# Optimization experiments

Measured on AMD Instinct MI355X. Metric: run time of the kernel, lower is better.

Reference implementation:

```python
import jax, jax.numpy as jnp
import numpy as np

RES_SIZE = 64
SR = 24000
MIN_FREQ = 10.0
MAX_FREQ = 12000.0
DECAY_FACTOR = 0.999
HIGH_FREQ_DECAY = 0.6


def _build_kernels():
    # Deterministic complex resonator bank from __init__ (registered buffer).
    freqs = np.logspace(np.log10(MIN_FREQ), np.log10(MAX_FREQ), RES_SIZE)
    decays = np.linspace(DECAY_FACTOR, HIGH_FREQ_DECAY, RES_SIZE)
    k_len = int(1.0 * SR)  # 24000
    t = np.arange(k_len)
    thetas = 2 * np.pi * freqs / SR
    eig = decays * np.exp(1j * thetas)  # (64,)
    kernels = eig[:, None] ** t[None, :]  # (64, 24000) complex
    kernels /= np.abs(kernels).sum(axis=1, keepdims=True)
    return kernels.astype(np.complex64)


def setup_inputs() -> dict:
    key = jax.random.key(0)
    audio = jax.random.normal(key, (8, 48000), dtype=jnp.float32)
    k = _build_kernels()
    return {
        "audio": audio,
        "kernels_re": jnp.asarray(k.real, dtype=jnp.float32),
        "kernels_im": jnp.asarray(k.imag, dtype=jnp.float32),
    }


def reference(audio, kernels_re, kernels_im):
    # audio: (B, T) float32; kernels: (C=64, K=24000) complex64 (as re/im pair)
    kernels = (kernels_re + 1j * kernels_im).astype(jnp.complex64)
    T = audio.shape[-1]
    K = kernels.shape[-1]
    n_fft = T + K - 1
    audio_c = audio.astype(jnp.complex64)

    ker_f = jnp.fft.fft(kernels, n=n_fft, axis=-1)[None, :, :]  # (1, C, n_fft)

    # forward-direction convolution
    sig_f = jnp.fft.fft(audio_c[:, None, :], n=n_fft, axis=-1)  # (B, 1, n_fft)
    out_f = jnp.fft.ifft(sig_f * ker_f, axis=-1)[..., :T]        # (B, C, T)

    # backward-direction convolution (time-reversed input, then re-reversed)
    sig_b = jnp.fft.fft(audio_c[:, ::-1][:, None, :], n=n_fft, axis=-1)
    out_b = jnp.fft.ifft(sig_b * ker_f, axis=-1)[..., :T][..., ::-1]

    # (B, 4*C, T): [RealF, ImagF, RealB, ImagB]
    return jnp.concatenate(
        [out_f.real, out_f.imag, out_b.real, out_b.imag], axis=1
    ).astype(jnp.float32)
```

## Files before the change

### kernel.cpp

```cpp
#include <hip/hip_runtime.h>

#define BATCH   8
#define NCH     64
#define TLEN    48000
#define KLEN    24000
#define NDIR    2
#define CHUNK   256
#define NCHUNK  188
#define NBD     (BATCH*NDIR)
#define NTASK_A (NBD*NCHUNK)
#define NTASK_C (NTASK_A*NCH)

#define WS_EIG_OFF ((size_t)NTASK_C * sizeof(float2))

__global__ __launch_bounds__(64) void pass0_eig(double* __restrict__ eig_out) {
    int c = threadIdx.x;
    if (c >= NCH) return;
    double fc  = (double)c / 63.0;
    double dec = 0.999 + (0.6 - 0.999) * fc;
    double lf  = 1.0 + (4.0791812460476247 - 1.0) * fc;
    double f   = pow(10.0, lf);
    double th  = 2.0 * 3.14159265358979323846 * f / 24000.0;
    eig_out[2 * c]     = dec * cos(th);
    eig_out[2 * c + 1] = dec * sin(th);
}

__global__ __launch_bounds__(256) void pass_a(const float* __restrict__ audio,
                                              const double* __restrict__ eig,
                                              float2* __restrict__ s_out) {
    int lane = threadIdx.x & 63;
    int task = blockIdx.x * 4 + (threadIdx.x >> 6);
    int chunk = task % NCHUNK;
    int bd    = task / NCHUNK;
    int d = bd & 1, b = bd >> 1;
    int c = lane;

    float er = (float)eig[2 * c], ei = (float)eig[2 * c + 1];
    float E2r = er * er - ei * ei, E2i = 2.f * er * ei;

    const float* ab = audio + b * TLEN;
    int base = chunk * CHUNK;
    int len  = min(CHUNK, TLEN - base);

    float sr = 0.f, si = 0.f;
    for (int t = 0; t < len; t += 2) {
        int u0 = base + t, u1 = base + t + 1;
        float x0 = ab[d ? (TLEN - 1 - u0) : u0];
        float x1 = ab[d ? (TLEN - 1 - u1) : u1];
        float wr = er * x0 + x1;
        float wi = ei * x0;
        float nr = E2r * sr - E2i * si + wr;
        float ni = E2r * si + E2i * sr + wi;
        sr = nr; si = ni;
    }
    s_out[task * NCH + c] = make_float2(sr, si);
}

__global__ __launch_bounds__(256) void pass_b(float2* __restrict__ buf,
                                              const double* __restrict__ eig) {
    int tid = blockIdx.x * 256 + threadIdx.x;
    if (tid >= NBD * NCH) return;
    int c  = tid & 63;
    int bd = tid >> 6;

    double er = eig[2 * c], ei = eig[2 * c + 1];
    double lr = er, li = ei;
    #pragma unroll
    for (int s = 0; s < 8; ++s) { double r = lr, i = li; lr = r * r - i * i; li = 2.0 * r * i; }

    double Sr = 0.0, Si = 0.0;
    #pragma unroll 4
    for (int i = 0; i < NCHUNK; ++i) {
        int idx = (bd * NCHUNK + i) * NCH + c;
        float2 s = buf[idx];
        buf[idx] = make_float2((float)Sr, (float)Si);
        double nr = lr * Sr - li * Si + (double)s.x;
        double ni = lr * Si + li * Sr + (double)s.y;
        Sr = nr; Si = ni;
    }
}

__global__ __launch_bounds__(256) void pass_c(const float* __restrict__ audio,
                                              const float* __restrict__ kre,
                                              const double* __restrict__ eig,
                                              const float2* __restrict__ S_in,
                                              float* __restrict__ out) {
    int lane = threadIdx.x & 63;
    int task = blockIdx.x * 4 + (threadIdx.x >> 6);
    int c     = task & 63;
    int tmp   = task >> 6;
    int chunk = tmp % NCHUNK;
    int bd    = tmp / NCHUNK;
    int d = bd & 1, b = bd >> 1;

    float Er[8], Ei[8];
    Er[0] = (float)eig[2 * c]; Ei[0] = (float)eig[2 * c + 1];
    #pragma unroll
    for (int s = 1; s < 8; ++s) {
        float r = Er[s - 1], i = Ei[s - 1];
        Er[s] = r * r - i * i; Ei[s] = 2.f * r * i;
    }
    float Qr = 1.f, Qi = 0.f;
    #pragma unroll
    for (int s = 0; s < 6; ++s) {
        float fr = Er[s + 2], fi = Ei[s + 2];
        float nr = Qr * fr - Qi * fi, ni = Qr * fi + Qi * fr;
        bool bit = (lane >> s) & 1;
        Qr = bit ? nr : Qr; Qi = bit ? ni : Qi;
    }
    float e1r = Er[0], e1i = Ei[0];
    float e2r = Er[1], e2i = Ei[1];
    float e3r = e1r * e2r - e1i * e2i, e3i = e1r * e2i + e1i * e2r;
    float e4r = Er[2], e4i = Ei[2];

    float  g  = kre[c * KLEN];
    float2 Sp = S_in[task];

    const float* ab = audio + b * TLEN;
    int base = chunk * CHUNK;
    int u    = base + 4 * lane;
    bool act = u < TLEN;

    float4 x;
    if (act) {
        if (!d) x = *(const float4*)(ab + u);
        else { float4 r = *(const float4*)(ab + (TLEN - 4 - u)); x = make_float4(r.w, r.z, r.y, r.x); }
    } else x = make_float4(0.f, 0.f, 0.f, 0.f);

    float z0r = x.x,                          z0i = 0.f;
    float z1r = e1r * z0r + x.y,              z1i = e1i * z0r;
    float z2r = e1r * z1r - e1i * z1i + x.z,  z2i = e1r * z1i + e1i * z1r;
    float z3r = e1r * z2r - e1i * z2i + x.w,  z3i = e1r * z2i + e1i * z2r;

    float Sr = z3r, Si = z3i;
    #pragma unroll
    for (int s = 0; s < 6; ++s) {
        float vr = __shfl_up(Sr, (unsigned)(1 << s), 64);
        float vi = __shfl_up(Si, (unsigned)(1 << s), 64);
        bool ok = lane >= (1 << s);
        vr = ok ? vr : 0.f; vi = ok ? vi : 0.f;
        float fr = Er[s + 2], fi = Ei[s + 2];
        Sr += fr * vr - fi * vi;
        Si += fr * vi + fi * vr;
    }
    float Cr = __shfl_up(Sr, 1u, 64), Ci = __shfl_up(Si, 1u, 64);
    if (lane == 0) { Cr = 0.f; Ci = 0.f; }
    float Dr = Cr + Qr * Sp.x - Qi * Sp.y;
    float Di = Ci + Qr * Sp.y + Qi * Sp.x;

    float y0r = z0r + e1r * Dr - e1i * Di, y0i = z0i + e1r * Di + e1i * Dr;
    float y1r = z1r + e2r * Dr - e2i * Di, y1i = z1i + e2r * Di + e2i * Dr;
    float y2r = z2r + e3r * Dr - e3i * Di, y2i = z2i + e3r * Di + e3i * Dr;
    float y3r = z3r + e4r * Dr - e4i * Di, y3i = z3i + e4r * Di + e4i * Dr;

    float* outR = out + (size_t)(b * 256 + d * 128 + c) * TLEN;
    float* outI = outR + (size_t)64 * TLEN;
    if (act) {
        if (!d) {
            *(float4*)(outR + u) = make_float4(g * y0r, g * y1r, g * y2r, g * y3r);
            *(float4*)(outI + u) = make_float4(g * y0i, g * y1i, g * y2i, g * y3i);
        } else {
            int p = TLEN - 4 - u;
            *(float4*)(outR + p) = make_float4(g * y3r, g * y2r, g * y1r, g * y0r);
            *(float4*)(outI + p) = make_float4(g * y3i, g * y2i, g * y1i, g * y0i);
        }
    }
}

extern "C" void kernel_launch(void* const* d_in, const int* in_sizes, int n_in,
                              void* d_out, int out_size, void* d_ws, size_t ws_size,
                              hipStream_t stream) {
    const float* audio = (const float*)d_in[0];
    const float* kre   = (const float*)d_in[1];
    float* out         = (float*)d_out;

    float2* ws_buf = (float2*)d_ws;
    double* ws_eig = (double*)((char*)d_ws + WS_EIG_OFF);

    pass0_eig<<<1, 64, 0, stream>>>(ws_eig);
    pass_a<<<NTASK_A / 4, 256, 0, stream>>>(audio, ws_eig, ws_buf);
    pass_b<<<(NBD * NCH + 255) / 256, 256, 0, stream>>>(ws_buf, ws_eig);
    pass_c<<<NTASK_C / 4, 256, 0, stream>>>(audio, kre, ws_eig, ws_buf, out);
}
```

Before: 453.6 us.

## Process four chunks per wave in pass_c with nontemporal output stores

Each pass_c wave now handles a super-chunk of four 256-sample chunks. It derives the carry-in for chunks 2-4 locally from the previous chunk's scan total and eig^256, so it no longer reads a separate carry per chunk. This spreads the eigen-power setup and the carry load over more work and gives each wave independent shuffle scans to interleave. Output writes use nontemporal stores to avoid polluting the cache with the large output, and pass_a's recurrence loop is unrolled. The costs are higher register pressure, a quarter as many waves, and some extra float rounding from chaining carries in single precision.

Result: faster. 437.8 us (-3.5%).

```diff
diff --git a/kernel.cpp b/kernel.cpp
--- a/kernel.cpp
+++ b/kernel.cpp
@@ -7,11 +7,21 @@
 #define NDIR    2
 #define CHUNK   256
 #define NCHUNK  188
+#define SUPER   4
+#define SCHUNK  (CHUNK*SUPER)
+#define NSUP    47
 #define NBD     (BATCH*NDIR)
 #define NTASK_A (NBD*NCHUNK)
-#define NTASK_C (NTASK_A*NCH)
-
-#define WS_EIG_OFF ((size_t)NTASK_C * sizeof(float2))
+#define NTASK_C (NBD*NSUP*NCH)
+
+#define WS_EIG_OFF ((size_t)(NTASK_A * NCH) * sizeof(float2))
+
+typedef float v4f __attribute__((ext_vector_type(4)));
+
+__device__ __forceinline__ void nt_store4(float* p, float a, float b, float c, float d) {
+    v4f v = {a, b, c, d};
+    __builtin_nontemporal_store(v, (v4f*)p);
+}
 
 __global__ __launch_bounds__(64) void pass0_eig(double* __restrict__ eig_out) {
     int c = threadIdx.x;
@@ -43,6 +53,7 @@
     int len  = min(CHUNK, TLEN - base);
 
     float sr = 0.f, si = 0.f;
+    #pragma unroll 4
     for (int t = 0; t < len; t += 2) {
         int u0 = base + t, u1 = base + t + 1;
         float x0 = ab[d ? (TLEN - 1 - u0) : u0];
@@ -87,10 +98,10 @@
                                               float* __restrict__ out) {
     int lane = threadIdx.x & 63;
     int task = blockIdx.x * 4 + (threadIdx.x >> 6);
-    int c     = task & 63;
-    int tmp   = task >> 6;
-    int chunk = tmp % NCHUNK;
-    int bd    = tmp / NCHUNK;
+    int c   = task & 63;
+    int tmp = task >> 6;
+    int sc  = tmp % NSUP;
+    int bd  = tmp / NSUP;
     int d = bd & 1, b = bd >> 1;
 
     float Er[8], Ei[8];
@@ -100,6 +111,9 @@
         float r = Er[s - 1], i = Ei[s - 1];
         Er[s] = r * r - i * i; Ei[s] = 2.f * r * i;
     }
+    float e256r = Er[7] * Er[7] - Ei[7] * Ei[7];
+    float e256i = 2.f * Er[7] * Ei[7];
+
     float Qr = 1.f, Qi = 0.f;
     #pragma unroll
     for (int s = 0; s < 6; ++s) {
@@ -114,55 +128,94 @@
     float e4r = Er[2], e4i = Ei[2];
 
     float  g  = kre[c * KLEN];
-    float2 Sp = S_in[task];
+    float2 Sp = S_in[(bd * NCHUNK + SUPER * sc) * NCH + c];
 
     const float* ab = audio + b * TLEN;
-    int base = chunk * CHUNK;
-    int u    = base + 4 * lane;
-    bool act = u < TLEN;
-
-    float4 x;
-    if (act) {
-        if (!d) x = *(const float4*)(ab + u);
-        else { float4 r = *(const float4*)(ab + (TLEN - 4 - u)); x = make_float4(r.w, r.z, r.y, r.x); }
-    } else x = make_float4(0.f, 0.f, 0.f, 0.f);
-
-    float z0r = x.x,                          z0i = 0.f;
-    float z1r = e1r * z0r + x.y,              z1i = e1i * z0r;
-    float z2r = e1r * z1r - e1i * z1i + x.z,  z2i = e1r * z1i + e1i * z1r;
-    float z3r = e1r * z2r - e1i * z2i + x.w,  z3i = e1r * z2i + e1i * z2r;
-
-    float Sr = z3r, Si = z3i;
+    int base0 = sc * SCHUNK;
+
+    float x0[SUPER], x1[SUPER], x2[SUPER], x3[SUPER];
+    bool  act[SUPER];
+    #pragma unroll
+    for (int j = 0; j < SUPER; ++j) {
+        int u = base0 + j * CHUNK + 4 * lane;
+        act[j] = (u < TLEN);
+        float4 x = make_float4(0.f, 0.f, 0.f, 0.f);
+        if (act[j]) {
+            if (!d) x = *(const float4*)(ab + u);
+            else { float4 r = *(const float4*)(ab + (TLEN - 4 - u)); x = make_float4(r.w, r.z, r.y, r.x); }
+        }
+        x0[j] = x.x; x1[j] = x.y; x2[j] = x.z; x3[j] = x.w;
+    }
+
+    float z0r[SUPER], z1r[SUPER], z1i[SUPER], z2r[SUPER], z2i[SUPER], z3r[SUPER], z3i[SUPER];
+    #pragma unroll
+    for (int j = 0; j < SUPER; ++j) {
+        z0r[j] = x0[j];
+        z1r[j] = e1r * z0r[j] + x1[j];
+        z1i[j] = e1i * z0r[j];
+        z2r[j] = e1r * z1r[j] - e1i * z1i[j] + x2[j];
+        z2i[j] = e1r * z1i[j] + e1i * z1r[j];
+        z3r[j] = e1r * z2r[j] - e1i * z2i[j] + x3[j];
+        z3i[j] = e1r * z2i[j] + e1i * z2r[j];
+    }
+
+    float Sr[SUPER], Si[SUPER];
+    #pragma unroll
+    for (int j = 0; j < SUPER; ++j) { Sr[j] = z3r[j]; Si[j] = z3i[j]; }
     #pragma unroll
     for (int s = 0; s < 6; ++s) {
-        float vr = __shfl_up(Sr, (unsigned)(1 << s), 64);
-        float vi = __shfl_up(Si, (unsigned)(1 << s), 64);
-        bool ok = lane >= (1 << s);
-        vr = ok ? vr : 0.f; vi = ok ? vi : 0.f;
         float fr = Er[s + 2], fi = Ei[s + 2];
-        Sr += fr * vr - fi * vi;
-        Si += fr * vi + fi * vr;
-    }
-    float Cr = __shfl_up(Sr, 1u, 64), Ci = __shfl_up(Si, 1u, 64);
-    if (lane == 0) { Cr = 0.f; Ci = 0.f; }
-    float Dr = Cr + Qr * Sp.x - Qi * Sp.y;
-    float Di = Ci + Qr * Sp.y + Qi * Sp.x;
-
-    float y0r = z0r + e1r * Dr - e1i * Di, y0i = z0i + e1r * Di + e1i * Dr;
-    float y1r = z1r + e2r * Dr - e2i * Di, y1i = z1i + e2r * Di + e2i * Dr;
-    float y2r = z2r + e3r * Dr - e3i * Di, y2i = z2i + e3r * Di + e3i * Dr;
-    float y3r = z3r + e4r * Dr - e4i * Di, y3i = z3i + e4r * Di + e4i * Dr;
+        #pragma unroll
+        for (int j = 0; j < SUPER; ++j) {
+            float vr = __shfl_up(Sr[j], (unsigned)(1 << s), 64);
+            float vi = __shfl_up(Si[j], (unsigned)(1 << s), 64);
+            bool ok = lane >= (1 << s);
+            vr = ok ? vr : 0.f; vi = ok ? vi : 0.f;
+            Sr[j] += fr * vr - fi * vi;
+            Si[j] += fr * vi + fi * vr;
+        }
+    }
+
+    float Cr[SUPER], Ci[SUPER], Tr[SUPER], Ti[SUPER];
+    #pragma unroll
+    for (int j = 0; j < SUPER; ++j) {
+        float cr = __shfl_up(Sr[j], 1u, 64), ci = __shfl_up(Si[j], 1u, 64);
+        Cr[j] = (lane == 0) ? 0.f : cr;
+        Ci[j] = (lane == 0) ? 0.f : ci;
+        Tr[j] = __shfl(Sr[j], 63, 64);
+        Ti[j] = __shfl(Si[j], 63, 64);
+    }
+
+    float Spr[SUPER], Spi[SUPER];
+    Spr[0] = Sp.x; Spi[0] = Sp.y;
+    #pragma unroll
+    for (int j = 1; j < SUPER; ++j) {
+        Spr[j] = e256r * Spr[j - 1] - e256i * Spi[j - 1] + Tr[j - 1];
+        Spi[j] = e256r * Spi[j - 1] + e256i * Spr[j - 1] + Ti[j - 1];
+    }
 
     float* outR = out + (size_t)(b * 256 + d * 128 + c) * TLEN;
     float* outI = outR + (size_t)64 * TLEN;
-    if (act) {
-        if (!d) {
-            *(float4*)(outR + u) = make_float4(g * y0r, g * y1r, g * y2r, g * y3r);
-            *(float4*)(outI + u) = make_float4(g * y0i, g * y1i, g * y2i, g * y3i);
-        } else {
-            int p = TLEN - 4 - u;
-            *(float4*)(outR + p) = make_float4(g * y3r, g * y2r, g * y1r, g * y0r);
-            *(float4*)(outI + p) = make_float4(g * y3i, g * y2i, g * y1i, g * y0i);
+    #pragma unroll
+    for (int j = 0; j < SUPER; ++j) {
+        float Dr = Cr[j] + Qr * Spr[j] - Qi * Spi[j];
+        float Di = Ci[j] + Qr * Spi[j] + Qi * Spr[j];
+
+        float y0r = z0r[j] + e1r * Dr - e1i * Di, y0i =          e1r * Di + e1i * Dr;
+        float y1r = z1r[j] + e2r * Dr - e2i * Di, y1i = z1i[j] + e2r * Di + e2i * Dr;
+        float y2r = z2r[j] + e3r * Dr - e3i * Di, y2i = z2i[j] + e3r * Di + e3i * Dr;
+        float y3r = z3r[j] + e4r * Dr - e4i * Di, y3i = z3i[j] + e4r * Di + e4i * Dr;
+
+        int u = base0 + j * CHUNK + 4 * lane;
+        if (act[j]) {
+            if (!d) {
+                nt_store4(outR + u, g * y0r, g * y1r, g * y2r, g * y3r);
+                nt_store4(outI + u, g * y0i, g * y1i, g * y2i, g * y3i);
+            } else {
+                int p = TLEN - 4 - u;
+                nt_store4(outR + p, g * y3r, g * y2r, g * y1r, g * y0r);
+                nt_store4(outI + p, g * y3i, g * y2i, g * y1i, g * y0i);
+            }
         }
     }
 }
```

## Parallelize chunk-carry scan with wave shuffles and widen pass_c to 1024-sample superchunks

Applied to the files above, without the earlier changes.

pass_b replaces the serial 188-step double-precision carry recurrence per (bd,channel) with a per-wave parallel scan: each lane handles three chunks and combines them through shuffle-based prefix steps using eigenvalue powers. pass_c now processes 1024-sample superchunks with 16 samples per lane, running a sequential recurrence in registers. It reuses every fourth chunk carry and writes output with nontemporal float4 stores. This is meant to remove pass_b's serial latency and cut per-task overhead and cache pollution in pass_c. In exchange the carries are computed in float rather than double, and longer in-register recurrences add dependency chains and some precision risk.

After: 971.1 us. 114% more time.

```diff
diff --git a/kernel.cpp b/kernel.cpp
--- a/kernel.cpp
+++ b/kernel.cpp
@@ -7,11 +7,20 @@
 #define NDIR    2
 #define CHUNK   256
 #define NCHUNK  188
+#define SCHUNK  1024
+#define NSUP    47
 #define NBD     (BATCH*NDIR)
 #define NTASK_A (NBD*NCHUNK)
-#define NTASK_C (NTASK_A*NCH)
-
-#define WS_EIG_OFF ((size_t)NTASK_C * sizeof(float2))
+#define NTASK_C (NBD*NSUP*NCH)
+
+#define WS_EIG_OFF ((size_t)(NTASK_A * NCH) * sizeof(float2))
+
+typedef float v4f __attribute__((ext_vector_type(4)));
+
+__device__ __forceinline__ void nt_store4(float* p, float a, float b, float c, float d) {
+    v4f v = {a, b, c, d};
+    __builtin_nontemporal_store(v, (v4f*)p);
+}
 
 __global__ __launch_bounds__(64) void pass0_eig(double* __restrict__ eig_out) {
     int c = threadIdx.x;
@@ -43,6 +52,7 @@
     int len  = min(CHUNK, TLEN - base);
 
     float sr = 0.f, si = 0.f;
+    #pragma unroll 4
     for (int t = 0; t < len; t += 2) {
         int u0 = base + t, u1 = base + t + 1;
         float x0 = ab[d ? (TLEN - 1 - u0) : u0];
@@ -58,26 +68,57 @@
 
 __global__ __launch_bounds__(256) void pass_b(float2* __restrict__ buf,
                                               const double* __restrict__ eig) {
-    int tid = blockIdx.x * 256 + threadIdx.x;
-    if (tid >= NBD * NCH) return;
-    int c  = tid & 63;
-    int bd = tid >> 6;
-
-    double er = eig[2 * c], ei = eig[2 * c + 1];
-    double lr = er, li = ei;
-    #pragma unroll
-    for (int s = 0; s < 8; ++s) { double r = lr, i = li; lr = r * r - i * i; li = 2.0 * r * i; }
-
-    double Sr = 0.0, Si = 0.0;
-    #pragma unroll 4
-    for (int i = 0; i < NCHUNK; ++i) {
-        int idx = (bd * NCHUNK + i) * NCH + c;
-        float2 s = buf[idx];
-        buf[idx] = make_float2((float)Sr, (float)Si);
-        double nr = lr * Sr - li * Si + (double)s.x;
-        double ni = lr * Si + li * Sr + (double)s.y;
-        Sr = nr; Si = ni;
-    }
+    int lane = threadIdx.x & 63;
+    int wv   = blockIdx.x * 4 + (threadIdx.x >> 6);
+    int c  = wv & 63;
+    int bd = wv >> 6;
+
+    double der = eig[2 * c], dei = eig[2 * c + 1];
+    #pragma unroll
+    for (int s = 0; s < 8; ++s) { double r = der, i = dei; der = r * r - i * i; dei = 2.0 * r * i; }
+    float ELr = (float)der, ELi = (float)dei;
+    double d2r = der * der - dei * dei, d2i = 2.0 * der * dei;
+    float EL2r = (float)d2r, EL2i = (float)d2i;
+    float EL3r = (float)(d2r * der - d2i * dei);
+    float EL3i = (float)(d2r * dei + d2i * der);
+
+    float Pr[6], Pi[6];
+    Pr[0] = EL3r; Pi[0] = EL3i;
+    #pragma unroll
+    for (int s = 1; s < 6; ++s) {
+        float r = Pr[s - 1], i = Pi[s - 1];
+        Pr[s] = r * r - i * i; Pi[s] = 2.f * r * i;
+    }
+
+    int i0 = 3 * lane;
+    float2 s0 = (i0     < NCHUNK) ? buf[(bd * NCHUNK + i0    ) * NCH + c] : make_float2(0.f, 0.f);
+    float2 s1 = (i0 + 1 < NCHUNK) ? buf[(bd * NCHUNK + i0 + 1) * NCH + c] : make_float2(0.f, 0.f);
+    float2 s2 = (i0 + 2 < NCHUNK) ? buf[(bd * NCHUNK + i0 + 2) * NCH + c] : make_float2(0.f, 0.f);
+
+    float Lr = EL2r * s0.x - EL2i * s0.y + ELr * s1.x - ELi * s1.y + s2.x;
+    float Li = EL2r * s0.y + EL2i * s0.x + ELr * s1.y + ELi * s1.x + s2.y;
+
+    float Sr = Lr, Si = Li;
+    #pragma unroll
+    for (int s = 0; s < 6; ++s) {
+        float vr = __shfl_up(Sr, (unsigned)(1 << s), 64);
+        float vi = __shfl_up(Si, (unsigned)(1 << s), 64);
+        bool ok = lane >= (1 << s);
+        vr = ok ? vr : 0.f; vi = ok ? vi : 0.f;
+        Sr += Pr[s] * vr - Pi[s] * vi;
+        Si += Pr[s] * vi + Pi[s] * vr;
+    }
+    float Cr = __shfl_up(Sr, 1u, 64), Ci = __shfl_up(Si, 1u, 64);
+    if (lane == 0) { Cr = 0.f; Ci = 0.f; }
+
+    float c0r = Cr, c0i = Ci;
+    if (i0 < NCHUNK) buf[(bd * NCHUNK + i0) * NCH + c] = make_float2(c0r, c0i);
+    float c1r = ELr * c0r - ELi * c0i + s0.x;
+    float c1i = ELr * c0i + ELi * c0r + s0.y;
+    if (i0 + 1 < NCHUNK) buf[(bd * NCHUNK + i0 + 1) * NCH + c] = make_float2(c1r, c1i);
+    float c2r = ELr * c1r - ELi * c1i + s1.x;
+    float c2i = ELr * c1i + ELi * c1r + s1.y;
+    if (i0 + 2 < NCHUNK) buf[(bd * NCHUNK + i0 + 2) * NCH + c] = make_float2(c2r, c2i);
 }
 
 __global__ __launch_bounds__(256) void pass_c(const float* __restrict__ audio,
@@ -87,59 +128,71 @@
                                               float* __restrict__ out) {
     int lane = threadIdx.x & 63;
     int task = blockIdx.x * 4 + (threadIdx.x >> 6);
-    int c     = task & 63;
-    int tmp   = task >> 6;
-    int chunk = tmp % NCHUNK;
-    int bd    = tmp / NCHUNK;
+    int c   = task & 63;
+    int tmp = task >> 6;
+    int sc  = tmp % NSUP;
+    int bd  = tmp / NSUP;
     int d = bd & 1, b = bd >> 1;
 
-    float Er[8], Ei[8];
+    float Er[10], Ei[10];
     Er[0] = (float)eig[2 * c]; Ei[0] = (float)eig[2 * c + 1];
     #pragma unroll
-    for (int s = 1; s < 8; ++s) {
+    for (int s = 1; s < 10; ++s) {
         float r = Er[s - 1], i = Ei[s - 1];
         Er[s] = r * r - i * i; Ei[s] = 2.f * r * i;
     }
+    float e1r = Er[0], e1i = Ei[0];
+
     float Qr = 1.f, Qi = 0.f;
     #pragma unroll
     for (int s = 0; s < 6; ++s) {
-        float fr = Er[s + 2], fi = Ei[s + 2];
+        float fr = Er[s + 4], fi = Ei[s + 4];
         float nr = Qr * fr - Qi * fi, ni = Qr * fi + Qi * fr;
         bool bit = (lane >> s) & 1;
         Qr = bit ? nr : Qr; Qi = bit ? ni : Qi;
     }
-    float e1r = Er[0], e1i = Ei[0];
-    float e2r = Er[1], e2i = Ei[1];
-    float e3r = e1r * e2r - e1i * e2i, e3i = e1r * e2i + e1i * e2r;
-    float e4r = Er[2], e4i = Ei[2];
 
     float  g  = kre[c * KLEN];
-    float2 Sp = S_in[task];
+    float2 Sp = S_in[(bd * NCHUNK + 4 * sc) * NCH + c];
 
     const float* ab = audio + b * TLEN;
-    int base = chunk * CHUNK;
-    int u    = base + 4 * lane;
-    bool act = u < TLEN;
-
-    float4 x;
-    if (act) {
-        if (!d) x = *(const float4*)(ab + u);
-        else { float4 r = *(const float4*)(ab + (TLEN - 4 - u)); x = make_float4(r.w, r.z, r.y, r.x); }
-    } else x = make_float4(0.f, 0.f, 0.f, 0.f);
-
-    float z0r = x.x,                          z0i = 0.f;
-    float z1r = e1r * z0r + x.y,              z1i = e1i * z0r;
-    float z2r = e1r * z1r - e1i * z1i + x.z,  z2i = e1r * z1i + e1i * z1r;
-    float z3r = e1r * z2r - e1i * z2i + x.w,  z3i = e1r * z2i + e1i * z2r;
-
-    float Sr = z3r, Si = z3i;
+    int base0 = sc * SCHUNK;
+    int u     = base0 + 16 * lane;
+    bool act  = u < TLEN;
+
+    float x[16];
+    #pragma unroll
+    for (int g4 = 0; g4 < 4; ++g4) {
+        float4 r = make_float4(0.f, 0.f, 0.f, 0.f);
+        if (act) {
+            if (!d) {
+                r = *(const float4*)(ab + u + 4 * g4);
+                x[4*g4+0] = r.x; x[4*g4+1] = r.y; x[4*g4+2] = r.z; x[4*g4+3] = r.w;
+            } else {
+                r = *(const float4*)(ab + (TLEN - 4 - u - 4 * g4));
+                x[4*g4+0] = r.w; x[4*g4+1] = r.z; x[4*g4+2] = r.y; x[4*g4+3] = r.x;
+            }
+        } else {
+            x[4*g4+0] = 0.f; x[4*g4+1] = 0.f; x[4*g4+2] = 0.f; x[4*g4+3] = 0.f;
+        }
+    }
+
+    float zr = x[0], zi = 0.f;
+    #pragma unroll
+    for (int k = 1; k < 16; ++k) {
+        float nr = e1r * zr - e1i * zi + x[k];
+        float ni = e1r * zi + e1i * zr;
+        zr = nr; zi = ni;
+    }
+
+    float Sr = zr, Si = zi;
     #pragma unroll
     for (int s = 0; s < 6; ++s) {
+        float fr = Er[s + 4], fi = Ei[s + 4];
         float vr = __shfl_up(Sr, (unsigned)(1 << s), 64);
         float vi = __shfl_up(Si, (unsigned)(1 << s), 64);
         bool ok = lane >= (1 << s);
         vr = ok ? vr : 0.f; vi = ok ? vi : 0.f;
-        float fr = Er[s + 2], fi = Ei[s + 2];
         Sr += fr * vr - fi * vi;
         Si += fr * vi + fi * vr;
     }
@@ -148,21 +201,29 @@
     float Dr = Cr + Qr * Sp.x - Qi * Sp.y;
     float Di = Ci + Qr * Sp.y + Qi * Sp.x;
 
-    float y0r = z0r + e1r * Dr - e1i * Di, y0i = z0i + e1r * Di + e1i * Dr;
-    float y1r = z1r + e2r * Dr - e2i * Di, y1i = z1i + e2r * Di + e2i * Dr;
-    float y2r = z2r + e3r * Dr - e3i * Di, y2i = z2i + e3r * Di + e3i * Dr;
-    float y3r = z3r + e4r * Dr - e4i * Di, y3i = z3i + e4r * Di + e4i * Dr;
-
     float* outR = out + (size_t)(b * 256 + d * 128 + c) * TLEN;
     float* outI = outR + (size_t)64 * TLEN;
-    if (act) {
-        if (!d) {
-            *(float4*)(outR + u) = make_float4(g * y0r, g * y1r, g * y2r, g * y3r);
-            *(float4*)(outI + u) = make_float4(g * y0i, g * y1i, g * y2i, g * y3i);
-        } else {
-            int p = TLEN - 4 - u;
-            *(float4*)(outR + p) = make_float4(g * y3r, g * y2r, g * y1r, g * y0r);
-            *(float4*)(outI + p) = make_float4(g * y3i, g * y2i, g * y1i, g * y0i);
+    float cr = Dr, ci = Di;
+    #pragma unroll
+    for (int g4 = 0; g4 < 4; ++g4) {
+        float yr[4], yi[4];
+        #pragma unroll
+        for (int m = 0; m < 4; ++m) {
+            int k = 4 * g4 + m;
+            float nr = e1r * cr - e1i * ci + x[k];
+            float ni = e1r * ci + e1i * cr;
+            cr = nr; ci = ni;
+            yr[m] = g * cr; yi[m] = g * ci;
+        }
+        if (act) {
+            if (!d) {
+                nt_store4(outR + u + 4 * g4, yr[0], yr[1], yr[2], yr[3]);
+                nt_store4(outI + u + 4 * g4, yi[0], yi[1], yi[2], yi[3]);
+            } else {
+                int p = TLEN - 4 - u - 4 * g4;
+                nt_store4(outR + p, yr[3], yr[2], yr[1], yr[0]);
+                nt_store4(outI + p, yi[3], yi[2], yi[1], yi[0]);
+            }
         }
     }
 }
@@ -179,6 +240,6 @@
 
     pass0_eig<<<1, 64, 0, stream>>>(ws_eig);
     pass_a<<<NTASK_A / 4, 256, 0, stream>>>(audio, ws_eig, ws_buf);
-    pass_b<<<(NBD * NCH + 255) / 256, 256, 0, stream>>>(ws_buf, ws_eig);
+    pass_b<<<(NBD * NCH) / 4, 256, 0, stream>>>(ws_buf, ws_eig);
     pass_c<<<NTASK_C / 4, 256, 0, stream>>>(audio, kre, ws_eig, ws_buf, out);
 }
```
